# Kernel optimization log

Measured on AMD Instinct MI355X. Metric: run time of the kernel, lower is better.

The kernel has to match this reference:

```python
import jax, jax.numpy as jnp
import numpy as np

NUM_CLASSES = 21
BBOX_NUM = 2
BG_CLASS = 20          # nums_classes - 1
NMS_THR = 0.5
CLASS_OFFSET = 4096.0  # batched-NMS trick: shift boxes per class so IoU across classes is 0


def setup_inputs() -> dict:
    key = jax.random.key(0)
    # post-backbone feature map: C = bbox_num*5 + num_classes = 31, 28x28 grid (stride-32 on 896 image)
    features = jax.random.normal(key, (64, 31, 28, 28), dtype=jnp.float32)
    return {"features": features, "h_ori": 896, "w_ori": 896}


def _pairwise_iou(b):
    # b: [N, 4] (x1, y1, x2, y2) -> [N, N] IoU
    x1 = jnp.maximum(b[:, None, 0], b[None, :, 0])
    y1 = jnp.maximum(b[:, None, 1], b[None, :, 1])
    x2 = jnp.minimum(b[:, None, 2], b[None, :, 2])
    y2 = jnp.minimum(b[:, None, 3], b[None, :, 3])
    inter = jnp.clip(x2 - x1, 0.0) * jnp.clip(y2 - y1, 0.0)
    area = jnp.clip(b[:, 2] - b[:, 0], 0.0) * jnp.clip(b[:, 3] - b[:, 1], 0.0)
    union = area[:, None] + area[None, :] - inter
    return inter / jnp.maximum(union, 1e-9)


def _nms(boxes, scores, cats, valid):
    # class-aware greedy NMS on a single image; returns bool keep mask [N]
    N = boxes.shape[0]
    obox = boxes + (cats.astype(boxes.dtype) * CLASS_OFFSET)[:, None]
    s = jnp.where(valid, scores, -jnp.inf)
    order = jnp.argsort(-s)                 # descending score
    iou = _pairwise_iou(obox[order])        # [N, N] among sorted boxes
    idx = jnp.arange(N)

    def body(i, keep):
        ki = keep[i]
        suppress = (iou[i] > NMS_THR) & (idx > i) & ki
        return keep & ~suppress

    keep_sorted = jax.lax.fori_loop(0, N, body, valid[order])
    return jnp.zeros(N, bool).at[order].set(keep_sorted)


def reference(features, h_ori, w_ori):
    B, C, Hf, Wf = features.shape
    N = Hf * Wf
    # permute_and_flatten: [B, C, H, W] -> [B, H*W, C]
    x = features.transpose(0, 2, 3, 1).reshape(B, N, C)

    con_idx = jnp.arange(4, BBOX_NUM * 5, 5)            # confidence channels
    pred_conf = x[:, :, con_idx]                        # [B, N, bbox_num]
    pred_bbox = jax.nn.sigmoid(x[:, :, :BBOX_NUM * 5])  # [B, N, bbox_num*5]
    pred_class = jax.nn.softmax(x[:, :, BBOX_NUM * 5:], axis=-1)  # [B, N, num_classes]

    conf_max = jnp.max(pred_conf, axis=-1)              # [B, N]
    conf_arg = jnp.argmax(pred_conf, axis=-1)           # [B, N]
    con_prob = conf_max[..., None] * pred_class
    prob = jnp.max(con_prob, axis=-1)                   # [B, N]
    cat = jnp.argmax(con_prob, axis=-1)                 # [B, N]

    # Boxer.filter_bboxes: gather the 4 coords of the max-confidence box (offset = argmax*5)
    gidx = (conf_arg * 5)[..., None] + jnp.arange(4)    # [B, N, 4]
    box = jnp.take_along_axis(pred_bbox, gidx, axis=-1) # (x, y, w, h) in grid units

    # grid_cell_2_bbox (inverse of config_gt encoding), cell idx = row*Wf + col
    col = (jnp.arange(N) % Wf).astype(box.dtype)
    row = (jnp.arange(N) // Wf).astype(box.dtype)
    cx = (box[..., 0] + col) * (w_ori / Wf)
    cy = (box[..., 1] + row) * (h_ori / Hf)
    bw = box[..., 2] * w_ori
    bh = box[..., 3] * h_ori
    # convert center xywh -> corners
    boxes = jnp.stack([cx - bw / 2, cy - bh / 2, cx + bw / 2, cy + bh / 2], axis=-1)

    valid = cat != BG_CLASS                             # background filtering
    keep = jax.vmap(_nms)(boxes, prob, cat, valid)      # per-image NMS

    # fixed-shape packed output: [x1, y1, x2, y2, prob, cat, keep] -> [B, N, 7]
    out = jnp.concatenate(
        [boxes, prob[..., None], cat.astype(jnp.float32)[..., None],
         jnp.where(keep, 1.0, 0.0)[..., None]], axis=-1)
    return out
```

## Files before the change

### kernel.cpp

```cpp
#include <hip/hip_runtime.h>

#define BATCH 64
#define CH 31
#define HF 28
#define WF 28
#define NCELL 784
#define NCLS 21
#define BGCLS 20
#define CAP 128
#define NMS_THR 0.5f

__device__ __forceinline__ float bcast_f(float v, int l) {
    return __int_as_float(__builtin_amdgcn_readlane(__float_as_int(v), l));
}

__global__ __launch_bounds__(256)
void decode_kernel(const float* __restrict__ feat,
                   const int* __restrict__ hofp,
                   const int* __restrict__ wofp,
                   float* __restrict__ out,
                   float4* __restrict__ wbox,
                   unsigned long long* __restrict__ wkey)
{
    int gid = blockIdx.x * blockDim.x + threadIdx.x;
    if (gid >= BATCH * NCELL) return;
    int b = gid / NCELL;
    int n = gid - b * NCELL;

    const float* base = feat + (size_t)b * CH * NCELL + n;
    float x[CH];
#pragma unroll
    for (int c = 0; c < CH; ++c) x[c] = base[(size_t)c * NCELL];

    float c0 = x[4], c1 = x[9];
    int carg = (c1 > c0) ? 1 : 0;
    float cmax = fmaxf(c0, c1);

    float m = x[10];
#pragma unroll
    for (int k = 1; k < NCLS; ++k) m = fmaxf(m, x[10 + k]);
    float e[NCLS];
    float sum = 0.0f;
#pragma unroll
    for (int k = 0; k < NCLS; ++k) { e[k] = expf(x[10 + k] - m); sum += e[k]; }
    float rinv = 1.0f / sum;

    float best = -INFINITY;
    int cat = 0;
#pragma unroll
    for (int k = 0; k < NCLS; ++k) {
        float cp = cmax * (e[k] * rinv);
        if (cp > best) { best = cp; cat = k; }
    }

    float rx = carg ? x[5] : x[0];
    float ry = carg ? x[6] : x[1];
    float rw = carg ? x[7] : x[2];
    float rh = carg ? x[8] : x[3];
    rx = 1.0f / (1.0f + expf(-rx));
    ry = 1.0f / (1.0f + expf(-ry));
    rw = 1.0f / (1.0f + expf(-rw));
    rh = 1.0f / (1.0f + expf(-rh));

    float w_ori = (float)(*wofp), h_ori = (float)(*hofp);
    float sw = w_ori / (float)WF, sh = h_ori / (float)HF;
    float col = (float)(n % WF), row = (float)(n / WF);
    float cx = (rx + col) * sw;
    float cy = (ry + row) * sh;
    float bw = rw * w_ori;
    float bh = rh * h_ori;
    float x1 = cx - bw * 0.5f, y1 = cy - bh * 0.5f;
    float x2 = cx + bw * 0.5f, y2 = cy + bh * 0.5f;

    float* o = out + (size_t)gid * 7;
    o[0] = x1; o[1] = y1; o[2] = x2; o[3] = y2;
    o[4] = best; o[5] = (float)cat; o[6] = 0.0f;

    float off = (float)cat * 4096.0f;
    wbox[gid] = make_float4(x1 + off, y1 + off, x2 + off, y2 + off);

    unsigned long long key = ~0ull;
    if (cat != BGCLS) {
        unsigned u = __float_as_uint(best);
        u = (u & 0x80000000u) ? ~u : (u | 0x80000000u);
        key = ((unsigned long long)(~u) << 15) |
              ((unsigned long long)cat << 10) | (unsigned)n;
    }
    wkey[gid] = key;
}

__global__ __launch_bounds__(64)
void nms_kernel(const float4* __restrict__ wbox,
                const unsigned long long* __restrict__ wkey,
                float* __restrict__ out)
{
    const int blk = blockIdx.x;
    const int b = blk / (NCLS - 1);
    const int c = blk - b * (NCLS - 1);
    const int lane = threadIdx.x;

    __shared__ unsigned long long lb[CAP];
    __shared__ unsigned long long lb2[CAP];

    int nacc = 0;
    const unsigned long long* wk = wkey + (size_t)b * NCELL;
#pragma unroll
    for (int it = 0; it < 13; ++it) {
        int cell = it * 64 + lane;
        bool m2 = false;
        unsigned long long key = ~0ull;
        if (cell < NCELL) {
            key = wk[cell];
            m2 = (((key >> 10) & 31ull) == (unsigned long long)c);
        }
        unsigned long long bal = __ballot(m2);
        if (m2) {
            int pos = nacc + __popcll(bal & ((1ull << lane) - 1ull));
            if (pos < CAP) lb[pos] = key;
        }
        nacc += (int)__popcll(bal);
    }
    int n = nacc > CAP ? CAP : nacc;
    if (n == 0) return;
    asm volatile("s_waitcnt lgkmcnt(0)" ::: "memory");

    bool ok0 = (lane < n);
    bool two = (n > 64);
    bool ok1 = two && ((64 + lane) < n);
    unsigned long long m0 = ok0 ? lb[lane] : ~0ull;
    unsigned long long m1 = ok1 ? lb[64 + lane] : ~0ull;

    int r0 = 0, r1 = 0;
    for (int j = 0; j < n; ++j) {
        unsigned long long kj = lb[j];
        r0 += (kj < m0) ? 1 : 0;
        r1 += (kj < m1) ? 1 : 0;
    }
    if (ok0) lb2[r0] = m0;
    if (ok1) lb2[r1] = m1;
    asm volatile("s_waitcnt lgkmcnt(0)" ::: "memory");

    unsigned long long k0 = ok0 ? lb2[lane] : ~0ull;
    unsigned long long k1 = ok1 ? lb2[64 + lane] : ~0ull;

    int cell0 = (int)(k0 & 1023ull);
    int cell1 = (int)(k1 & 1023ull);

    const float4* wb = wbox + (size_t)b * NCELL;
    float4 B0 = wb[ok0 ? cell0 : 0];
    float a0 = fmaxf(B0.z - B0.x, 0.f) * fmaxf(B0.w - B0.y, 0.f);
    float4 B1 = make_float4(0.f, 0.f, 0.f, 0.f);
    float a1 = 0.f;
    if (two) {
        B1 = wb[ok1 ? cell1 : 0];
        a1 = fmaxf(B1.z - B1.x, 0.f) * fmaxf(B1.w - B1.y, 0.f);
    }

    unsigned long long keep0 = (n >= 64) ? ~0ull : ((1ull << n) - 1);
    unsigned long long keep1 = two ? ((n >= 128) ? ~0ull : ((1ull << (n - 64)) - 1))
                                   : 0ull;

    unsigned long long rem = keep0;
    while (rem) {
        int i = __builtin_ctzll(rem);
        rem &= rem - 1;
        float ix1 = bcast_f(B0.x, i), iy1 = bcast_f(B0.y, i);
        float ix2 = bcast_f(B0.z, i), iy2 = bcast_f(B0.w, i);
        float ia  = bcast_f(a0, i);
        {
            float xx1 = fmaxf(ix1, B0.x), yy1 = fmaxf(iy1, B0.y);
            float xx2 = fminf(ix2, B0.z), yy2 = fminf(iy2, B0.w);
            float inter = fmaxf(xx2 - xx1, 0.f) * fmaxf(yy2 - yy1, 0.f);
            float uni = ia + a0 - inter;
            bool s = (inter / fmaxf(uni, 1e-9f)) > NMS_THR;
            unsigned long long mm = __ballot(s) & keep0;
            mm &= (i < 63) ? (~0ull << (i + 1)) : 0ull;
            keep0 &= ~mm; rem &= ~mm;
        }
        if (two) {
            float xx1 = fmaxf(ix1, B1.x), yy1 = fmaxf(iy1, B1.y);
            float xx2 = fminf(ix2, B1.z), yy2 = fminf(iy2, B1.w);
            float inter = fmaxf(xx2 - xx1, 0.f) * fmaxf(yy2 - yy1, 0.f);
            float uni = ia + a1 - inter;
            bool s = (inter / fmaxf(uni, 1e-9f)) > NMS_THR;
            keep1 &= ~(__ballot(s) & keep1);
        }
    }
    if (two) {
        unsigned long long rem1 = keep1;
        while (rem1) {
            int i = __builtin_ctzll(rem1);
            rem1 &= rem1 - 1;
            float ix1 = bcast_f(B1.x, i), iy1 = bcast_f(B1.y, i);
            float ix2 = bcast_f(B1.z, i), iy2 = bcast_f(B1.w, i);
            float ia  = bcast_f(a1, i);
            float xx1 = fmaxf(ix1, B1.x), yy1 = fmaxf(iy1, B1.y);
            float xx2 = fminf(ix2, B1.z), yy2 = fminf(iy2, B1.w);
            float inter = fmaxf(xx2 - xx1, 0.f) * fmaxf(yy2 - yy1, 0.f);
            float uni = ia + a1 - inter;
            bool s = (inter / fmaxf(uni, 1e-9f)) > NMS_THR;
            unsigned long long mm = __ballot(s) & keep1;
            mm &= (i < 63) ? (~0ull << (i + 1)) : 0ull;
            keep1 &= ~mm; rem1 &= ~mm;
        }
    }

    if (ok0 && ((keep0 >> lane) & 1ull))
        out[((size_t)b * NCELL + cell0) * 7 + 6] = 1.0f;
    if (ok1 && ((keep1 >> lane) & 1ull))
        out[((size_t)b * NCELL + cell1) * 7 + 6] = 1.0f;
}

extern "C" void kernel_launch(void* const* d_in, const int* in_sizes, int n_in,
                              void* d_out, int out_size, void* d_ws, size_t ws_size,
                              hipStream_t stream) {
    const float* feat = (const float*)d_in[0];
    const int* h_ori  = (const int*)d_in[1];
    const int* w_ori  = (const int*)d_in[2];
    float* out = (float*)d_out;

    float4* wbox = (float4*)d_ws;
    unsigned long long* wkey =
        (unsigned long long*)((char*)d_ws + sizeof(float4) * BATCH * NCELL);

    int total = BATCH * NCELL;
    decode_kernel<<<(total + 255) / 256, 256, 0, stream>>>(
        feat, h_ori, w_ori, out, wbox, wkey);
    nms_kernel<<<BATCH * (NCLS - 1), 64, 0, stream>>>(wbox, wkey, out);
}
```

Measured before the change: 25.21 us.

## Precompute IoU suppression bitmasks before serial NMS sweep and vectorize key loads

The NMS kernel now computes every pairwise IoU up front, with no data dependence, and stores the results as per-lane bitmasks. The greedy sweep then reduces to ballot and mask operations instead of evaluating IoU inside the serial chain. Key compaction and the rank-sort loop read two 64-bit keys per load, and the shared buffer is pre-filled with sentinel keys so the sort can run over pairs. The trade-off is that IoU is now computed for all pairs rather than only for surviving boxes, which adds work when many boxes get suppressed.

After: 26.12 us. 3.6% more time.

```diff
diff --git a/kernel.cpp b/kernel.cpp
--- a/kernel.cpp
+++ b/kernel.cpp
@@ -99,26 +99,33 @@
     const int c = blk - b * (NCLS - 1);
     const int lane = threadIdx.x;
 
-    __shared__ unsigned long long lb[CAP];
+    __shared__ alignas(16) unsigned long long lb[CAP];
     __shared__ unsigned long long lb2[CAP];
 
+    lb[lane] = ~0ull;
+    lb[64 + lane] = ~0ull;
+
     int nacc = 0;
-    const unsigned long long* wk = wkey + (size_t)b * NCELL;
-#pragma unroll
-    for (int it = 0; it < 13; ++it) {
-        int cell = it * 64 + lane;
-        bool m2 = false;
-        unsigned long long key = ~0ull;
-        if (cell < NCELL) {
-            key = wk[cell];
-            m2 = (((key >> 10) & 31ull) == (unsigned long long)c);
-        }
-        unsigned long long bal = __ballot(m2);
-        if (m2) {
-            int pos = nacc + __popcll(bal & ((1ull << lane) - 1ull));
-            if (pos < CAP) lb[pos] = key;
-        }
-        nacc += (int)__popcll(bal);
+    const ulonglong2* wk2 =
+        (const ulonglong2*)(wkey + (size_t)b * NCELL);
+    unsigned long long low = (lane == 0) ? 0ull : ((1ull << lane) - 1ull);
+#pragma unroll
+    for (int it = 0; it < 7; ++it) {
+        int ci = it * 128 + 2 * lane;
+        unsigned long long ke = ~0ull, ko = ~0ull;
+        if (ci < NCELL) {
+            ulonglong2 kk = wk2[it * 64 + lane];
+            ke = kk.x; ko = kk.y;
+        }
+        bool me = (((ke >> 10) & 31ull) == (unsigned long long)c);
+        bool mo = (((ko >> 10) & 31ull) == (unsigned long long)c);
+        unsigned long long balE = __ballot(me);
+        unsigned long long balO = __ballot(mo);
+        int pe = nacc + __popcll(balE & low) + __popcll(balO & low);
+        int po = pe + (int)((balE >> lane) & 1ull);
+        if (me && pe < CAP) lb[pe] = ke;
+        if (mo && po < CAP) lb[po] = ko;
+        nacc += (int)(__popcll(balE) + __popcll(balO));
     }
     int n = nacc > CAP ? CAP : nacc;
     if (n == 0) return;
@@ -127,14 +134,16 @@
     bool ok0 = (lane < n);
     bool two = (n > 64);
     bool ok1 = two && ((64 + lane) < n);
-    unsigned long long m0 = ok0 ? lb[lane] : ~0ull;
-    unsigned long long m1 = ok1 ? lb[64 + lane] : ~0ull;
+    unsigned long long m0 = lb[lane];
+    unsigned long long m1 = lb[64 + lane];
 
     int r0 = 0, r1 = 0;
-    for (int j = 0; j < n; ++j) {
-        unsigned long long kj = lb[j];
-        r0 += (kj < m0) ? 1 : 0;
-        r1 += (kj < m1) ? 1 : 0;
+    const ulonglong2* lp = (const ulonglong2*)lb;
+    int half = (n + 1) >> 1;
+    for (int j = 0; j < half; ++j) {
+        ulonglong2 kk = lp[j];
+        r0 += (kk.x < m0) ? 1 : 0; r0 += (kk.y < m0) ? 1 : 0;
+        r1 += (kk.x < m1) ? 1 : 0; r1 += (kk.y < m1) ? 1 : 0;
     }
     if (ok0) lb2[r0] = m0;
     if (ok1) lb2[r1] = m1;
@@ -142,7 +151,6 @@
 
     unsigned long long k0 = ok0 ? lb2[lane] : ~0ull;
     unsigned long long k1 = ok1 ? lb2[64 + lane] : ~0ull;
-
     int cell0 = (int)(k0 & 1023ull);
     int cell1 = (int)(k1 & 1023ull);
 
@@ -156,52 +164,63 @@
         a1 = fmaxf(B1.z - B1.x, 0.f) * fmaxf(B1.w - B1.y, 0.f);
     }
 
-    unsigned long long keep0 = (n >= 64) ? ~0ull : ((1ull << n) - 1);
-    unsigned long long keep1 = two ? ((n >= 128) ? ~0ull : ((1ull << (n - 64)) - 1))
-                                   : 0ull;
-
-    unsigned long long rem = keep0;
-    while (rem) {
-        int i = __builtin_ctzll(rem);
-        rem &= rem - 1;
-        float ix1 = bcast_f(B0.x, i), iy1 = bcast_f(B0.y, i);
-        float ix2 = bcast_f(B0.z, i), iy2 = bcast_f(B0.w, i);
-        float ia  = bcast_f(a0, i);
+    unsigned long long s00 = 0ull, s01 = 0ull, s11 = 0ull;
+    int n0 = (n < 64) ? n : 64;
+    for (int s = 0; s < n0; ++s) {
+        float ix1 = bcast_f(B0.x, s), iy1 = bcast_f(B0.y, s);
+        float ix2 = bcast_f(B0.z, s), iy2 = bcast_f(B0.w, s);
+        float ia  = bcast_f(a0, s);
         {
             float xx1 = fmaxf(ix1, B0.x), yy1 = fmaxf(iy1, B0.y);
             float xx2 = fminf(ix2, B0.z), yy2 = fminf(iy2, B0.w);
             float inter = fmaxf(xx2 - xx1, 0.f) * fmaxf(yy2 - yy1, 0.f);
             float uni = ia + a0 - inter;
-            bool s = (inter / fmaxf(uni, 1e-9f)) > NMS_THR;
-            unsigned long long mm = __ballot(s) & keep0;
-            mm &= (i < 63) ? (~0ull << (i + 1)) : 0ull;
-            keep0 &= ~mm; rem &= ~mm;
+            if ((inter / fmaxf(uni, 1e-9f)) > NMS_THR) s00 |= (1ull << s);
         }
         if (two) {
             float xx1 = fmaxf(ix1, B1.x), yy1 = fmaxf(iy1, B1.y);
             float xx2 = fminf(ix2, B1.z), yy2 = fminf(iy2, B1.w);
             float inter = fmaxf(xx2 - xx1, 0.f) * fmaxf(yy2 - yy1, 0.f);
             float uni = ia + a1 - inter;
-            bool s = (inter / fmaxf(uni, 1e-9f)) > NMS_THR;
-            keep1 &= ~(__ballot(s) & keep1);
-        }
+            if ((inter / fmaxf(uni, 1e-9f)) > NMS_THR) s01 |= (1ull << s);
+        }
+    }
+    if (two) {
+        int n1 = n - 64;
+        for (int s = 0; s < n1; ++s) {
+            float ix1 = bcast_f(B1.x, s), iy1 = bcast_f(B1.y, s);
+            float ix2 = bcast_f(B1.z, s), iy2 = bcast_f(B1.w, s);
+            float ia  = bcast_f(a1, s);
+            float xx1 = fmaxf(ix1, B1.x), yy1 = fmaxf(iy1, B1.y);
+            float xx2 = fminf(ix2, B1.z), yy2 = fminf(iy2, B1.w);
+            float inter = fmaxf(xx2 - xx1, 0.f) * fmaxf(yy2 - yy1, 0.f);
+            float uni = ia + a1 - inter;
+            if ((inter / fmaxf(uni, 1e-9f)) > NMS_THR) s11 |= (1ull << s);
+        }
+    }
+    unsigned long long tri = (lane == 0) ? 0ull : ((1ull << lane) - 1ull);
+    s00 &= tri;
+    s11 &= tri;
+
+    unsigned long long keep0 = (n >= 64) ? ~0ull : ((1ull << n) - 1ull);
+    unsigned long long keep1 =
+        two ? ((n >= 128) ? ~0ull : ((1ull << (n - 64)) - 1ull)) : 0ull;
+
+    unsigned long long rem = keep0;
+    while (rem) {
+        int i = __builtin_ctzll(rem);
+        rem &= rem - 1ull;
+        keep0 &= ~__ballot(((s00 >> i) & 1ull) != 0ull);
+        if (two) keep1 &= ~__ballot(((s01 >> i) & 1ull) != 0ull);
+        rem &= keep0;
     }
     if (two) {
         unsigned long long rem1 = keep1;
         while (rem1) {
             int i = __builtin_ctzll(rem1);
-            rem1 &= rem1 - 1;
-            float ix1 = bcast_f(B1.x, i), iy1 = bcast_f(B1.y, i);
-            float ix2 = bcast_f(B1.z, i), iy2 = bcast_f(B1.w, i);
-            float ia  = bcast_f(a1, i);
-            float xx1 = fmaxf(ix1, B1.x), yy1 = fmaxf(iy1, B1.y);
-            float xx2 = fminf(ix2, B1.z), yy2 = fminf(iy2, B1.w);
-            float inter = fmaxf(xx2 - xx1, 0.f) * fmaxf(yy2 - yy1, 0.f);
-            float uni = ia + a1 - inter;
-            bool s = (inter / fmaxf(uni, 1e-9f)) > NMS_THR;
-            unsigned long long mm = __ballot(s) & keep1;
-            mm &= (i < 63) ? (~0ull << (i + 1)) : 0ull;
-            keep1 &= ~mm; rem1 &= ~mm;
+            rem1 &= rem1 - 1ull;
+            keep1 &= ~__ballot(((s11 >> i) & 1ull) != 0ull);
+            rem1 &= keep1;
         }
     }
 
```
